# Optimization experiments

Measured on AMD Instinct MI355X. Metric: run time of the kernel, lower is better.

Reference implementation:

```python
import jax, jax.numpy as jnp
import numpy as np

HID = 256
E = 2 * HID  # 512, attention embed dim
H = 2        # attention heads


def _lin(x, w, b):
    return x @ w.T + b


def setup_inputs() -> dict:
    key = jax.random.key(0)
    ks = jax.random.split(key, 16)
    N, Ng, G = 65536, 4096, 16
    s = 0.02
    def w(k, o, i):
        return jax.random.normal(k, (o, i), jnp.float32) * s
    return {
        "flat_pair_enc": jax.random.normal(ks[0], (N, E), jnp.float32),
        "flat_pair_encA": jax.random.normal(ks[1], (N, E + 2), jnp.float32),
        "attn_in_w": w(ks[2], 3 * E, E), "attn_in_b": jnp.zeros(3 * E, jnp.float32),
        "attn_out_w": w(ks[3], E, E), "attn_out_b": jnp.zeros(E, jnp.float32),
        "phi1_w1": w(ks[4], HID, E + 2), "phi1_b1": jnp.zeros(HID, jnp.float32),
        "phi1_w2": w(ks[5], HID, HID), "phi1_b2": jnp.zeros(HID, jnp.float32),
        "phi1_w3": w(ks[6], HID, HID), "phi1_b3": jnp.zeros(HID, jnp.float32),
        "phi1_w4": w(ks[7], E, HID), "phi1_b4": jnp.zeros(E, jnp.float32),
        "g_w1": w(ks[8], HID, E), "g_b1": jnp.zeros(HID, jnp.float32),
        "g_w2": w(ks[9], HID, HID), "g_b2": jnp.zeros(HID, jnp.float32),
        "g_w3": w(ks[10], HID, HID), "g_b3": jnp.zeros(HID, jnp.float32),
        "g_w4": w(ks[11], 1, HID), "g_b4": jnp.zeros(1, jnp.float32),
        "phi2_w1": w(ks[12], HID, E), "phi2_b1": jnp.zeros(HID, jnp.float32),
        "phi2_w2": w(ks[13], HID, HID), "phi2_b2": jnp.zeros(HID, jnp.float32),
        "phi2_w3": w(ks[14], 2, HID), "phi2_b3": jnp.zeros(2, jnp.float32),
        "num_groups": 4096,
        "group_size": 16,
    }


def reference(flat_pair_enc, flat_pair_encA,
              attn_in_w, attn_in_b, attn_out_w, attn_out_b,
              phi1_w1, phi1_b1, phi1_w2, phi1_b2, phi1_w3, phi1_b3, phi1_w4, phi1_b4,
              g_w1, g_b1, g_w2, g_b2, g_w3, g_b3, g_w4, g_b4,
              phi2_w1, phi2_b1, phi2_w2, phi2_b2, phi2_w3, phi2_b3,
              num_groups, group_size):
    elu = jax.nn.elu
    Ng, G = num_groups, group_size
    # phi1 (note the double ELU after the second Linear, as in the source)
    h = elu(_lin(flat_pair_encA, phi1_w1, phi1_b1))
    h = elu(elu(_lin(h, phi1_w2, phi1_b2)))
    h = elu(_lin(h, phi1_w3, phi1_b3))
    key1 = _lin(h, phi1_w4, phi1_b4)                      # (N, E)
    x = key1.reshape(Ng, G, E)                            # segmented groups
    # per-group MultiheadAttention (torch semantics: packed in_proj, scale 1/sqrt(dh))
    qkv = x @ attn_in_w.T + attn_in_b                     # (Ng, G, 3E)
    q, k, v = jnp.split(qkv, 3, axis=-1)
    dh = E // H
    def heads(t):
        return t.reshape(Ng, G, H, dh).transpose(0, 2, 1, 3)  # (Ng, H, G, dh)
    q, k, v = heads(q), heads(k), heads(v)
    scores = jnp.einsum('nhqd,nhkd->nhqk', q, k) / jnp.sqrt(jnp.float32(dh))
    a = jax.nn.softmax(scores, axis=-1)
    o = jnp.einsum('nhqk,nhkd->nhqd', a, v).transpose(0, 2, 1, 3).reshape(Ng, G, E)
    key1_mean = (o @ attn_out_w.T + attn_out_b).mean(axis=1)  # (Ng, E) — mean over seq
    # g head
    hg = elu(_lin(key1_mean, g_w1, g_b1))
    hg = elu(_lin(hg, g_w2, g_b2))
    hg = elu(_lin(hg, g_w3, g_b3))
    q_jt = _lin(hg, g_w4, g_b4)                           # (Ng, 1)
    # alt values: k2 + kbar1 - key1/|g|  (counts per group == G)
    alt_val = flat_pair_enc.reshape(Ng, G, E) + key1_mean[:, None, :] - x / G
    hp = elu(_lin(alt_val, phi2_w1, phi2_b1))
    hp = elu(_lin(hp, phi2_w2, phi2_b2))
    alt_q = _lin(hp, phi2_w3, phi2_b3)                    # (Ng, G, 2)
    return (q_jt, alt_q)
```

## Files before the change

kernel.cpp:

```cpp
#include <hip/hip_runtime.h>
#include <cstdint>

typedef __bf16 bf16;
typedef __attribute__((ext_vector_type(8))) __bf16 bf16x8;
typedef __attribute__((ext_vector_type(4))) __bf16 bf16x4;
typedef __attribute__((ext_vector_type(4))) float f32x4;
typedef __attribute__((ext_vector_type(2))) float f32x2;

static __device__ __forceinline__ float elu1(float x) {
    return x > 0.f ? x : (__expf(x) - 1.f);
}

static __device__ __forceinline__ void gl_lds16(const void* gp, void* lp) {
    __builtin_amdgcn_global_load_lds(
        (const __attribute__((address_space(1))) void*)(uintptr_t)gp,
        (__attribute__((address_space(3))) void*)(uint32_t)(uintptr_t)lp,
        16, 0, 0);
}

struct CvtArgs {
    const float* src[13];
    int rows[13];
    int scols[13];
    int dcols[13];
    int total;
};

__global__ void cvt_k(CvtArgs a, bf16* __restrict__ dst) {
    int idx = blockIdx.x * 256 + threadIdx.x;
    if (idx >= a.total) return;
    int rem = idx;
#pragma unroll 1
    for (int s = 0; s < 13; ++s) {
        int sz = a.rows[s] * a.dcols[s];
        if (rem < sz) {
            int r = rem / a.dcols[s];
            int c = rem - r * a.dcols[s];
            float v = (c < a.scols[s]) ? a.src[s][(long)r * a.scols[s] + c] : 0.f;
            dst[idx] = (bf16)v;
            return;
        }
        rem -= sz;
    }
}

__global__ void cvtA_k(const float* __restrict__ src, bf16* __restrict__ dst) {
    const int idx = blockIdx.x * 256 + threadIdx.x;
    const int r = idx / 72;
    const int c8 = (idx - r * 72) * 8;
    const float* sp = src + (long)r * 514 + c8;
    bf16x8 t;
    if (c8 + 8 <= 514) {
        f32x2 p0 = *(const f32x2*)(sp + 0);
        f32x2 p1 = *(const f32x2*)(sp + 2);
        f32x2 p2 = *(const f32x2*)(sp + 4);
        f32x2 p3 = *(const f32x2*)(sp + 6);
        t[0] = (bf16)p0.x; t[1] = (bf16)p0.y; t[2] = (bf16)p1.x; t[3] = (bf16)p1.y;
        t[4] = (bf16)p2.x; t[5] = (bf16)p2.y; t[6] = (bf16)p3.x; t[7] = (bf16)p3.y;
    } else {
#pragma unroll
        for (int e = 0; e < 8; ++e) {
            const int col = c8 + e;
            t[e] = (bf16)(col < 514 ? sp[e] : 0.f);
        }
    }
    *(bf16x8*)(dst + (long)r * 576 + c8) = t;
}

struct GemmArgs {
    const float* Af;
    const bf16*  Ab;
    long lda;
    const float* enc;
    const float* km;
    const bf16*  key1;
    const bf16*  W;
    long ldw;
    const float* bias;
    bf16*  Cb;
    float* Cf;
    long ldc;
    int nK;
    int klim;
};

enum { AM_F32 = 0, AM_F32U = 1, AM_BF16 = 2, AM_ALT = 3 };
enum { ACT_NONE = 0, ACT_ELU = 1, ACT_ELU2 = 2 };

template <int AMODE, int ACT, bool OUTB>
__global__ __launch_bounds__(256, 2) void gemm_t(GemmArgs g) {
    __shared__ bf16 As[128 * 64];
    __shared__ bf16 Bs[128 * 64];

    const int tid  = threadIdx.x;
    const int wave = tid >> 6;
    const int lane = tid & 63;
    const int ln   = lane & 15;
    const int quad = lane >> 4;

    const long m0 = (long)blockIdx.x * 128;
    const long n0 = (long)blockIdx.y * 128;
    const int  wm = (wave & 1) * 64;
    const int  wn = (wave >> 1) * 64;

    f32x4 acc[4][4] = {};

    int cm[4], cs[4];
    long ar[4];
    if constexpr (AMODE != AM_BF16) {
#pragma unroll
        for (int r = 0; r < 4; ++r) {
            const int c = r * 256 + tid;
            cm[r] = c >> 3;
            cs[r] = c & 7;
            ar[r] = m0 + cm[r];
        }
    }

    f32x4 pf[4][2];
    float pu[4][8];
    f32x4 pe[4][2], pq[4][2];
    bf16x8 px[4];

    auto loadA = [&](int k0) {
#pragma unroll
        for (int r = 0; r < 4; ++r) {
            const int kk = k0 + (((cs[r] - cm[r]) & 7) << 3);
            if constexpr (AMODE == AM_F32) {
                const float* ap = g.Af + ar[r] * g.lda + kk;
                pf[r][0] = *(const f32x4*)ap;
                pf[r][1] = *(const f32x4*)(ap + 4);
            } else if constexpr (AMODE == AM_F32U) {
                const float* ap = g.Af + ar[r] * g.lda;
                if (kk + 8 <= g.klim) {
#pragma unroll
                    for (int e = 0; e < 8; e += 2) {
                        f32x2 p = *(const f32x2*)(ap + kk + e);
                        pu[r][e] = p.x;
                        pu[r][e + 1] = p.y;
                    }
                } else {
#pragma unroll
                    for (int e = 0; e < 8; ++e) {
                        const int col = kk + e;
                        pu[r][e] = col < g.klim ? ap[col] : 0.f;
                    }
                }
            } else if constexpr (AMODE == AM_ALT) {
                const float* ep = g.enc + ar[r] * 512 + kk;
                const float* mp = g.km + (ar[r] >> 4) * 512 + kk;
                pe[r][0] = *(const f32x4*)ep;
                pe[r][1] = *(const f32x4*)(ep + 4);
                pq[r][0] = *(const f32x4*)mp;
                pq[r][1] = *(const f32x4*)(mp + 4);
                px[r] = *(const bf16x8*)(g.key1 + ar[r] * 512 + kk);
            }
        }
    };

    auto writeA = [&]() {
#pragma unroll
        for (int r = 0; r < 4; ++r) {
            bf16x8 t;
            if constexpr (AMODE == AM_F32) {
#pragma unroll
                for (int e = 0; e < 4; ++e) {
                    t[e]     = (bf16)pf[r][0][e];
                    t[e + 4] = (bf16)pf[r][1][e];
                }
            } else if constexpr (AMODE == AM_F32U) {
#pragma unroll
                for (int e = 0; e < 8; ++e) t[e] = (bf16)pu[r][e];
            } else {
#pragma unroll
                for (int e = 0; e < 4; ++e) {
                    t[e]     = (bf16)(pe[r][0][e] + pq[r][0][e] - (float)px[r][e] * 0.0625f);
                    t[e + 4] = (bf16)(pe[r][1][e] + pq[r][1][e] - (float)px[r][e + 4] * 0.0625f);
                }
            }
            *(bf16x8*)(&As[cm[r] * 64 + cs[r] * 8]) = t;
        }
    };

    if constexpr (AMODE != AM_BF16) loadA(0);

    for (int ks = 0; ks < g.nK; ++ks) {
        const int k0 = ks * 64;
        __syncthreads();

        if constexpr (AMODE == AM_BF16) {
            const int cbase = wave * 256;
#pragma unroll
            for (int r = 0; r < 4; ++r) {
                const int c = cbase + r * 64 + lane;
                const int m = c >> 3, s = c & 7;
                const int pg = (s - m) & 7;
                gl_lds16(g.Ab + (m0 + m) * g.lda + k0 + pg * 8, &As[c * 8]);
            }
        } else {
            writeA();
        }

        {
            const int cbase = wave * 256;
#pragma unroll
            for (int r = 0; r < 4; ++r) {
                const int c = cbase + r * 64 + lane;
                const int n = c >> 3, s = c & 7;
                const int pg = (s - n) & 7;
                gl_lds16(g.W + (n0 + n) * g.ldw + k0 + pg * 8, &Bs[c * 8]);
            }
        }
        __syncthreads();

        if constexpr (AMODE != AM_BF16) {
            if (ks + 1 < g.nK) loadA(k0 + 64);
        }

#pragma unroll
        for (int ksub = 0; ksub < 2; ++ksub) {
            bf16x8 av[4], bv[4];
#pragma unroll
            for (int t = 0; t < 4; ++t) {
                const int m = wm + t * 16 + ln;
                const int sa = ((ksub * 4 + quad) + m) & 7;
                av[t] = *(const bf16x8*)(&As[m * 64 + sa * 8]);
                const int n = wn + t * 16 + ln;
                const int sb = ((ksub * 4 + quad) + n) & 7;
                bv[t] = *(const bf16x8*)(&Bs[n * 64 + sb * 8]);
            }
#pragma unroll
            for (int i = 0; i < 4; ++i)
#pragma unroll
                for (int j = 0; j < 4; ++j)
                    acc[i][j] = __builtin_amdgcn_mfma_f32_16x16x32_bf16(
                        av[i], bv[j], acc[i][j], 0, 0, 0);
        }
    }

#pragma unroll
    for (int i = 0; i < 4; ++i) {
        const long rb = m0 + wm + i * 16 + quad * 4;
#pragma unroll
        for (int j = 0; j < 4; ++j) {
            const long n = n0 + wn + j * 16 + ln;
            const float bvs = g.bias[n];
#pragma unroll
            for (int r = 0; r < 4; ++r) {
                float v = acc[i][j][r] + bvs;
                if constexpr (ACT >= ACT_ELU) v = elu1(v);
                if constexpr (ACT == ACT_ELU2) v = elu1(v);
                const long o = (rb + r) * g.ldc + n;
                if constexpr (OUTB) g.Cb[o] = (bf16)v;
                else                g.Cf[o] = v;
            }
        }
    }
}

__global__ __launch_bounds__(256) void attn_k(const bf16* __restrict__ qkv,
                                              bf16* __restrict__ obar,
                                              int ngroups) {
    const int tid = blockIdx.x * 256 + threadIdx.x;
    const int wv = tid >> 6;
    const int g  = wv >> 1;
    const int h  = wv & 1;
    if (g >= ngroups) return;
    const int lane = threadIdx.x & 63;
    const int i  = lane & 15;
    const int jb = (lane >> 4) << 2;

    const bf16* base  = qkv + (long)g * 16 * 1536;
    const bf16* qrow  = base + (long)i * 1536 + h * 256;
    const bf16* kbase = base + 512 + h * 256;

    float s0 = 0.f, s1 = 0.f, s2 = 0.f, s3 = 0.f;
    for (int kk = 0; kk < 256; kk += 8) {
        bf16x8 qv = *(const bf16x8*)(qrow + kk);
        float qf[8];
#pragma unroll
        for (int e = 0; e < 8; ++e) qf[e] = (float)qv[e];
        bf16x8 k0 = *(const bf16x8*)(kbase + (long)(jb + 0) * 1536 + kk);
        bf16x8 k1 = *(const bf16x8*)(kbase + (long)(jb + 1) * 1536 + kk);
        bf16x8 k2 = *(const bf16x8*)(kbase + (long)(jb + 2) * 1536 + kk);
        bf16x8 k3 = *(const bf16x8*)(kbase + (long)(jb + 3) * 1536 + kk);
#pragma unroll
        for (int e = 0; e < 8; ++e) {
            s0 += qf[e] * (float)k0[e];
            s1 += qf[e] * (float)k1[e];
            s2 += qf[e] * (float)k2[e];
            s3 += qf[e] * (float)k3[e];
        }
    }
    const float sc = 1.f / 16.f;
    s0 *= sc; s1 *= sc; s2 *= sc; s3 *= sc;
    float m = fmaxf(fmaxf(s0, s1), fmaxf(s2, s3));
    m = fmaxf(m, __shfl_xor(m, 16));
    m = fmaxf(m, __shfl_xor(m, 32));
    float e0 = __expf(s0 - m), e1 = __expf(s1 - m), e2 = __expf(s2 - m), e3 = __expf(s3 - m);
    float rs = e0 + e1 + e2 + e3;
    rs += __shfl_xor(rs, 16);
    rs += __shfl_xor(rs, 32);
    const float inv = 1.f / (rs * 16.f);
    float cb[4] = {e0 * inv, e1 * inv, e2 * inv, e3 * inv};
#pragma unroll
    for (int msk = 1; msk <= 8; msk <<= 1) {
        cb[0] += __shfl_xor(cb[0], msk);
        cb[1] += __shfl_xor(cb[1], msk);
        cb[2] += __shfl_xor(cb[2], msk);
        cb[3] += __shfl_xor(cb[3], msk);
    }
    float call[16];
#pragma unroll
    for (int j = 0; j < 16; ++j)
        call[j] = __shfl(cb[j & 3], (j >> 2) << 4);

    const int d0 = lane << 2;
    const bf16* vb = base + 1024 + h * 256 + d0;
    float o0 = 0.f, o1 = 0.f, o2 = 0.f, o3 = 0.f;
#pragma unroll
    for (int j = 0; j < 16; ++j) {
        bf16x4 vv = *(const bf16x4*)(vb + (long)j * 1536);
        o0 += call[j] * (float)vv[0];
        o1 += call[j] * (float)vv[1];
        o2 += call[j] * (float)vv[2];
        o3 += call[j] * (float)vv[3];
    }
    bf16x4 ov;
    ov[0] = (bf16)o0; ov[1] = (bf16)o1; ov[2] = (bf16)o2; ov[3] = (bf16)o3;
    *(bf16x4*)(obar + (long)g * 512 + h * 256 + d0) = ov;
}

__global__ void qjt_k(const bf16* __restrict__ hg, const bf16* __restrict__ w,
                      const float* __restrict__ b, float* __restrict__ out) {
    const int m = blockIdx.x * 256 + threadIdx.x;
    const bf16* hp = hg + (long)m * 256;
    float acc = 0.f;
    for (int k = 0; k < 256; k += 8) {
        bf16x8 hv = *(const bf16x8*)(hp + k);
        bf16x8 wv = *(const bf16x8*)(w + k);
#pragma unroll
        for (int e = 0; e < 8; ++e) acc += (float)hv[e] * (float)wv[e];
    }
    out[m] = acc + b[0];
}

__global__ void altq_k(const bf16* __restrict__ hp, const bf16* __restrict__ w,
                       const float* __restrict__ b, float* __restrict__ out) {
    const int m = blockIdx.x * 256 + threadIdx.x;
    const bf16* hr = hp + (long)m * 256;
    float a0 = 0.f, a1 = 0.f;
    for (int k = 0; k < 256; k += 8) {
        bf16x8 hv = *(const bf16x8*)(hr + k);
        bf16x8 w0 = *(const bf16x8*)(w + k);
        bf16x8 w1 = *(const bf16x8*)(w + 256 + k);
#pragma unroll
        for (int e = 0; e < 8; ++e) {
            float hf = (float)hv[e];
            a0 += hf * (float)w0[e];
            a1 += hf * (float)w1[e];
        }
    }
    out[2 * m]     = a0 + b[0];
    out[2 * m + 1] = a1 + b[1];
}

extern "C" void kernel_launch(void* const* d_in, const int* in_sizes, int n_in,
                              void* d_out, int out_size, void* d_ws, size_t ws_size,
                              hipStream_t stream) {
    const float* enc    = (const float*)d_in[0];
    const float* encA   = (const float*)d_in[1];
    const float* w_ain  = (const float*)d_in[2];
    const float* b_ain  = (const float*)d_in[3];
    const float* w_aout = (const float*)d_in[4];
    const float* b_aout = (const float*)d_in[5];
    const float* w_p11  = (const float*)d_in[6];
    const float* b_p11  = (const float*)d_in[7];
    const float* w_p12  = (const float*)d_in[8];
    const float* b_p12  = (const float*)d_in[9];
    const float* w_p13  = (const float*)d_in[10];
    const float* b_p13  = (const float*)d_in[11];
    const float* w_p14  = (const float*)d_in[12];
    const float* b_p14  = (const float*)d_in[13];
    const float* w_g1   = (const float*)d_in[14];
    const float* b_g1   = (const float*)d_in[15];
    const float* w_g2   = (const float*)d_in[16];
    const float* b_g2   = (const float*)d_in[17];
    const float* w_g3   = (const float*)d_in[18];
    const float* b_g3   = (const float*)d_in[19];
    const float* w_g4   = (const float*)d_in[20];
    const float* b_g4   = (const float*)d_in[21];
    const float* w_p21  = (const float*)d_in[22];
    const float* b_p21  = (const float*)d_in[23];
    const float* w_p22  = (const float*)d_in[24];
    const float* b_p22  = (const float*)d_in[25];
    const float* w_p23  = (const float*)d_in[26];
    const float* b_p23  = (const float*)d_in[27];
    float* out = (float*)d_out;

    char* wsc = (char*)d_ws;
    size_t off = 0;
    auto take = [&](size_t bytes) -> char* {
        char* p = wsc + off;
        off += (bytes + 255) & ~(size_t)255;
        return p;
    };

    const long o_ain  = 0;
    const long o_aout = o_ain + 1536L * 512;
    const long o_p11  = o_aout + 512L * 512;
    const long o_p12  = o_p11 + 256L * 576;
    const long o_p13  = o_p12 + 256L * 256;
    const long o_p14  = o_p13 + 256L * 256;
    const long o_g1   = o_p14 + 512L * 256;
    const long o_g2   = o_g1 + 256L * 512;
    const long o_g3   = o_g2 + 256L * 256;
    const long o_g4   = o_g3 + 256L * 256;
    const long o_p21  = o_g4 + 256L;
    const long o_p22  = o_p21 + 256L * 512;
    const long o_p23  = o_p22 + 256L * 256;
    const long wtot   = o_p23 + 2L * 256;

    bf16*  wb  = (bf16*)take((size_t)wtot * 2);
    bf16*  Ha  = (bf16*)take(65536ull * 256 * 2);
    bf16*  Hb  = (bf16*)take(65536ull * 256 * 2);
    bf16*  K1  = (bf16*)take(65536ull * 512 * 2);
    bf16*  OB  = (bf16*)take(4096ull * 512 * 2);
    float* KM  = (float*)take(4096ull * 512 * 4);
    bf16*  HGa = (bf16*)take(4096ull * 256 * 2);
    bf16*  HGb = (bf16*)take(4096ull * 256 * 2);

    const size_t apad_b = 65536ull * 576 * 2;
    const size_t avail = ws_size > off ? ws_size - off : 0;
    bool apad_ok = apad_b <= avail;
    auto qkvb = [](int ch) { return (size_t)(65536 / ch) * 1536 * 2; };
    auto need = [&](size_t q) {
        const size_t a = apad_ok ? apad_b : 0;
        return q > a ? q : a;
    };
    int CH = 16;
    if (need(qkvb(2)) <= avail)      CH = 2;
    else if (need(qkvb(4)) <= avail) CH = 4;
    else if (need(qkvb(8)) <= avail) CH = 8;
    else {
        CH = 16;
        if (need(qkvb(16)) > avail) apad_ok = false;
    }
    bf16* U = (bf16*)take(need(qkvb(CH)));
    bf16* Apad = U;
    bf16* QKV  = U;

    CvtArgs ca;
    const float* srcs[13] = {w_ain, w_aout, w_p11, w_p12, w_p13, w_p14,
                             w_g1, w_g2, w_g3, w_g4, w_p21, w_p22, w_p23};
    const int rows_[13]  = {1536, 512, 256, 256, 256, 512, 256, 256, 256, 1, 256, 256, 2};
    const int scols_[13] = {512, 512, 514, 256, 256, 256, 512, 256, 256, 256, 512, 256, 256};
    const int dcols_[13] = {512, 512, 576, 256, 256, 256, 512, 256, 256, 256, 512, 256, 256};
    for (int s = 0; s < 13; ++s) {
        ca.src[s] = srcs[s]; ca.rows[s] = rows_[s];
        ca.scols[s] = scols_[s]; ca.dcols[s] = dcols_[s];
    }
    ca.total = (int)wtot;
    cvt_k<<<dim3((unsigned)((wtot + 255) / 256)), dim3(256), 0, stream>>>(ca, wb);
    if (apad_ok)
        cvtA_k<<<dim3(18432), dim3(256), 0, stream>>>(encA, Apad);

    GemmArgs ga;

    if (apad_ok) {
        ga = {}; ga.Ab = Apad; ga.lda = 576;
        ga.W = wb + o_p11; ga.ldw = 576; ga.bias = b_p11;
        ga.Cb = Ha; ga.ldc = 256; ga.nK = 9;
        gemm_t<AM_BF16, ACT_ELU, true><<<dim3(512, 2), 256, 0, stream>>>(ga);
    } else {
        ga = {}; ga.Af = encA; ga.lda = 514; ga.klim = 514;
        ga.W = wb + o_p11; ga.ldw = 576; ga.bias = b_p11;
        ga.Cb = Ha; ga.ldc = 256; ga.nK = 9;
        gemm_t<AM_F32U, ACT_ELU, true><<<dim3(512, 2), 256, 0, stream>>>(ga);
    }

    ga = {}; ga.Ab = Ha; ga.lda = 256; ga.W = wb + o_p12; ga.ldw = 256;
    ga.bias = b_p12; ga.Cb = Hb; ga.ldc = 256; ga.nK = 4;
    gemm_t<AM_BF16, ACT_ELU2, true><<<dim3(512, 2), 256, 0, stream>>>(ga);

    ga = {}; ga.Ab = Hb; ga.lda = 256; ga.W = wb + o_p13; ga.ldw = 256;
    ga.bias = b_p13; ga.Cb = Ha; ga.ldc = 256; ga.nK = 4;
    gemm_t<AM_BF16, ACT_ELU, true><<<dim3(512, 2), 256, 0, stream>>>(ga);

    ga = {}; ga.Ab = Ha; ga.lda = 256; ga.W = wb + o_p14; ga.ldw = 256;
    ga.bias = b_p14; ga.Cb = K1; ga.ldc = 512; ga.nK = 4;
    gemm_t<AM_BF16, ACT_NONE, true><<<dim3(512, 4), 256, 0, stream>>>(ga);

    const int Mc = 65536 / CH;
    const int gc = 4096 / CH;
    for (int c = 0; c < CH; ++c) {
        ga = {}; ga.Ab = K1 + (long)c * Mc * 512; ga.lda = 512;
        ga.W = wb + o_ain; ga.ldw = 512; ga.bias = b_ain;
        ga.Cb = QKV; ga.ldc = 1536; ga.nK = 8;
        gemm_t<AM_BF16, ACT_NONE, true>
            <<<dim3(Mc / 128, 12), 256, 0, stream>>>(ga);
        attn_k<<<dim3((gc * 2) / 4), 256, 0, stream>>>(QKV, OB + (long)c * gc * 512, gc);
    }

    ga = {}; ga.Ab = OB; ga.lda = 512; ga.W = wb + o_aout; ga.ldw = 512;
    ga.bias = b_aout; ga.Cf = KM; ga.ldc = 512; ga.nK = 8;
    gemm_t<AM_BF16, ACT_NONE, false><<<dim3(32, 4), 256, 0, stream>>>(ga);

    ga = {}; ga.Af = KM; ga.lda = 512; ga.W = wb + o_g1; ga.ldw = 512;
    ga.bias = b_g1; ga.Cb = HGa; ga.ldc = 256; ga.nK = 8;
    gemm_t<AM_F32, ACT_ELU, true><<<dim3(32, 2), 256, 0, stream>>>(ga);

    ga = {}; ga.Ab = HGa; ga.lda = 256; ga.W = wb + o_g2; ga.ldw = 256;
    ga.bias = b_g2; ga.Cb = HGb; ga.ldc = 256; ga.nK = 4;
    gemm_t<AM_BF16, ACT_ELU, true><<<dim3(32, 2), 256, 0, stream>>>(ga);

    ga = {}; ga.Ab = HGb; ga.lda = 256; ga.W = wb + o_g3; ga.ldw = 256;
    ga.bias = b_g3; ga.Cb = HGa; ga.ldc = 256; ga.nK = 4;
    gemm_t<AM_BF16, ACT_ELU, true><<<dim3(32, 2), 256, 0, stream>>>(ga);

    qjt_k<<<dim3(16), 256, 0, stream>>>(HGa, wb + o_g4, b_g4, out);

    ga = {}; ga.enc = enc; ga.km = KM; ga.key1 = K1;
    ga.W = wb + o_p21; ga.ldw = 512; ga.bias = b_p21;
    ga.Cb = Ha; ga.ldc = 256; ga.nK = 8;
    gemm_t<AM_ALT, ACT_ELU, true><<<dim3(512, 2), 256, 0, stream>>>(ga);

    ga = {}; ga.Ab = Ha; ga.lda = 256; ga.W = wb + o_p22; ga.ldw = 256;
    ga.bias = b_p22; ga.Cb = Hb; ga.ldc = 256; ga.nK = 4;
    gemm_t<AM_BF16, ACT_ELU, true><<<dim3(512, 2), 256, 0, stream>>>(ga);

    altq_k<<<dim3(256), 256, 0, stream>>>(Hb, wb + o_p23, b_p23, out + 4096);
}
```

Baseline: 787.5 us.

## Double-buffer LDS tiles in GEMM to overlap loads with MFMA

```diff
diff --git a/kernel.cpp b/kernel.cpp
--- a/kernel.cpp
+++ b/kernel.cpp
@@ -89,8 +89,8 @@
 
 template <int AMODE, int ACT, bool OUTB>
 __global__ __launch_bounds__(256, 2) void gemm_t(GemmArgs g) {
-    __shared__ bf16 As[128 * 64];
-    __shared__ bf16 Bs[128 * 64];
+    __shared__ bf16 As[2][128 * 64];
+    __shared__ bf16 Bs[2][128 * 64];
 
     const int tid  = threadIdx.x;
     const int wave = tid >> 6;
@@ -158,7 +158,7 @@
         }
     };
 
-    auto writeA = [&]() {
+    auto writeA = [&](int b) {
 #pragma unroll
         for (int r = 0; r < 4; ++r) {
             bf16x8 t;
@@ -178,43 +178,59 @@
                     t[e + 4] = (bf16)(pe[r][1][e] + pq[r][1][e] - (float)px[r][e + 4] * 0.0625f);
                 }
             }
-            *(bf16x8*)(&As[cm[r] * 64 + cs[r] * 8]) = t;
+            *(bf16x8*)(&As[b][cm[r] * 64 + cs[r] * 8]) = t;
         }
     };
 
-    if constexpr (AMODE != AM_BF16) loadA(0);
-
+    auto stageA = [&](int ks, int b) {
+        const int cbase = wave * 256;
+        const int k0 = ks * 64;
+#pragma unroll
+        for (int r = 0; r < 4; ++r) {
+            const int c = cbase + r * 64 + lane;
+            const int m = c >> 3, s = c & 7;
+            const int pg = (s - m) & 7;
+            gl_lds16(g.Ab + (m0 + m) * g.lda + k0 + pg * 8, &As[b][c * 8]);
+        }
+    };
+
+    auto stageB = [&](int ks, int b) {
+        const int cbase = wave * 256;
+        const int k0 = ks * 64;
+#pragma unroll
+        for (int r = 0; r < 4; ++r) {
+            const int c = cbase + r * 64 + lane;
+            const int n = c >> 3, s = c & 7;
+            const int pg = (s - n) & 7;
+            gl_lds16(g.W + (n0 + n) * g.ldw + k0 + pg * 8, &Bs[b][c * 8]);
+        }
+    };
+
+    if constexpr (AMODE == AM_BF16) {
+        stageA(0, 0);
+    } else {
+        loadA(0);
+        writeA(0);
+    }
+    stageB(0, 0);
+    if constexpr (AMODE != AM_BF16) {
+        if (g.nK > 1) loadA(64);
+    }
+
+    int cur = 0;
     for (int ks = 0; ks < g.nK; ++ks) {
-        const int k0 = ks * 64;
         __syncthreads();
 
-        if constexpr (AMODE == AM_BF16) {
-            const int cbase = wave * 256;
-#pragma unroll
-            for (int r = 0; r < 4; ++r) {
-                const int c = cbase + r * 64 + lane;
-                const int m = c >> 3, s = c & 7;
-                const int pg = (s - m) & 7;
-                gl_lds16(g.Ab + (m0 + m) * g.lda + k0 + pg * 8, &As[c * 8]);
+        if (ks + 1 < g.nK) {
+            if constexpr (AMODE == AM_BF16) {
+                stageA(ks + 1, cur ^ 1);
+            } else {
+                writeA(cur ^ 1);
             }
-        } else {
-            writeA();
-        }
-
-        {
-            const int cbase = wave * 256;
-#pragma unroll
-            for (int r = 0; r < 4; ++r) {
-                const int c = cbase + r * 64 + lane;
-                const int n = c >> 3, s = c & 7;
-                const int pg = (s - n) & 7;
-                gl_lds16(g.W + (n0 + n) * g.ldw + k0 + pg * 8, &Bs[c * 8]);
+            stageB(ks + 1, cur ^ 1);
+            if constexpr (AMODE != AM_BF16) {
+                if (ks + 2 < g.nK) loadA((ks + 2) * 64);
             }
-        }
-        __syncthreads();
-
-        if constexpr (AMODE != AM_BF16) {
-            if (ks + 1 < g.nK) loadA(k0 + 64);
         }
 
 #pragma unroll
@@ -224,10 +240,10 @@
             for (int t = 0; t < 4; ++t) {
                 const int m = wm + t * 16 + ln;
                 const int sa = ((ksub * 4 + quad) + m) & 7;
-                av[t] = *(const bf16x8*)(&As[m * 64 + sa * 8]);
+                av[t] = *(const bf16x8*)(&As[cur][m * 64 + sa * 8]);
                 const int n = wn + t * 16 + ln;
                 const int sb = ((ksub * 4 + quad) + n) & 7;
-                bv[t] = *(const bf16x8*)(&Bs[n * 64 + sb * 8]);
+                bv[t] = *(const bf16x8*)(&Bs[cur][n * 64 + sb * 8]);
             }
 #pragma unroll
             for (int i = 0; i < 4; ++i)
@@ -236,6 +252,7 @@
                     acc[i][j] = __builtin_amdgcn_mfma_f32_16x16x32_bf16(
                         av[i], bv[j], acc[i][j], 0, 0, 0);
         }
+        cur ^= 1;
     }
 
 #pragma unroll
```

Measured after the change: 810.0 us. 2.9% more time.

## Double-buffer GEMM LDS tiles to overlap next-tile staging with MFMA compute

Applied to the files above, without the earlier changes.

```diff
diff --git a/kernel.cpp b/kernel.cpp
--- a/kernel.cpp
+++ b/kernel.cpp
@@ -89,8 +89,10 @@
 
 template <int AMODE, int ACT, bool OUTB>
 __global__ __launch_bounds__(256, 2) void gemm_t(GemmArgs g) {
-    __shared__ bf16 As[128 * 64];
-    __shared__ bf16 Bs[128 * 64];
+    __shared__ bf16 As0[128 * 64];
+    __shared__ bf16 As1[128 * 64];
+    __shared__ bf16 Bs0[128 * 64];
+    __shared__ bf16 Bs1[128 * 64];
 
     const int tid  = threadIdx.x;
     const int wave = tid >> 6;
@@ -158,7 +160,7 @@
         }
     };
 
-    auto writeA = [&]() {
+    auto writeA = [&](bf16 (&Ad)[128 * 64]) {
 #pragma unroll
         for (int r = 0; r < 4; ++r) {
             bf16x8 t;
@@ -178,45 +180,35 @@
                     t[e + 4] = (bf16)(pe[r][1][e] + pq[r][1][e] - (float)px[r][e + 4] * 0.0625f);
                 }
             }
-            *(bf16x8*)(&As[cm[r] * 64 + cs[r] * 8]) = t;
-        }
-    };
-
-    if constexpr (AMODE != AM_BF16) loadA(0);
-
-    for (int ks = 0; ks < g.nK; ++ks) {
+            *(bf16x8*)(&Ad[cm[r] * 64 + cs[r] * 8]) = t;
+        }
+    };
+
+    auto stageA = [&](int ks, bf16 (&Ad)[128 * 64]) {
+        const int cbase = wave * 256;
         const int k0 = ks * 64;
-        __syncthreads();
-
-        if constexpr (AMODE == AM_BF16) {
-            const int cbase = wave * 256;
-#pragma unroll
-            for (int r = 0; r < 4; ++r) {
-                const int c = cbase + r * 64 + lane;
-                const int m = c >> 3, s = c & 7;
-                const int pg = (s - m) & 7;
-                gl_lds16(g.Ab + (m0 + m) * g.lda + k0 + pg * 8, &As[c * 8]);
-            }
-        } else {
-            writeA();
-        }
-
-        {
-            const int cbase = wave * 256;
-#pragma unroll
-            for (int r = 0; r < 4; ++r) {
-                const int c = cbase + r * 64 + lane;
-                const int n = c >> 3, s = c & 7;
-                const int pg = (s - n) & 7;
-                gl_lds16(g.W + (n0 + n) * g.ldw + k0 + pg * 8, &Bs[c * 8]);
-            }
-        }
-        __syncthreads();
-
-        if constexpr (AMODE != AM_BF16) {
-            if (ks + 1 < g.nK) loadA(k0 + 64);
-        }
-
+#pragma unroll
+        for (int r = 0; r < 4; ++r) {
+            const int c = cbase + r * 64 + lane;
+            const int m = c >> 3, s = c & 7;
+            const int pg = (s - m) & 7;
+            gl_lds16(g.Ab + (m0 + m) * g.lda + k0 + pg * 8, &Ad[c * 8]);
+        }
+    };
+
+    auto stageB = [&](int ks, bf16 (&Bd)[128 * 64]) {
+        const int cbase = wave * 256;
+        const int k0 = ks * 64;
+#pragma unroll
+        for (int r = 0; r < 4; ++r) {
+            const int c = cbase + r * 64 + lane;
+            const int n = c >> 3, s = c & 7;
+            const int pg = (s - n) & 7;
+            gl_lds16(g.W + (n0 + n) * g.ldw + k0 + pg * 8, &Bd[c * 8]);
+        }
+    };
+
+    auto computeT = [&](const bf16 (&Ab_)[128 * 64], const bf16 (&Bb_)[128 * 64]) {
 #pragma unroll
         for (int ksub = 0; ksub < 2; ++ksub) {
             bf16x8 av[4], bv[4];
@@ -224,10 +216,10 @@
             for (int t = 0; t < 4; ++t) {
                 const int m = wm + t * 16 + ln;
                 const int sa = ((ksub * 4 + quad) + m) & 7;
-                av[t] = *(const bf16x8*)(&As[m * 64 + sa * 8]);
+                av[t] = *(const bf16x8*)(&Ab_[m * 64 + sa * 8]);
                 const int n = wn + t * 16 + ln;
                 const int sb = ((ksub * 4 + quad) + n) & 7;
-                bv[t] = *(const bf16x8*)(&Bs[n * 64 + sb * 8]);
+                bv[t] = *(const bf16x8*)(&Bb_[n * 64 + sb * 8]);
             }
 #pragma unroll
             for (int i = 0; i < 4; ++i)
@@ -236,6 +228,44 @@
                     acc[i][j] = __builtin_amdgcn_mfma_f32_16x16x32_bf16(
                         av[i], bv[j], acc[i][j], 0, 0, 0);
         }
+    };
+
+    if constexpr (AMODE == AM_BF16) {
+        stageA(0, As0);
+    } else {
+        loadA(0);
+        writeA(As0);
+    }
+    stageB(0, Bs0);
+    if constexpr (AMODE != AM_BF16) {
+        if (g.nK > 1) loadA(64);
+    }
+
+    const int nK = g.nK;
+    for (int ks = 0;;) {
+        __syncthreads();
+        if (ks + 1 < nK) {
+            if constexpr (AMODE == AM_BF16) stageA(ks + 1, As1);
+            else                            writeA(As1);
+            stageB(ks + 1, Bs1);
+            if constexpr (AMODE != AM_BF16) {
+                if (ks + 2 < nK) loadA((ks + 2) * 64);
+            }
+        }
+        computeT(As0, Bs0);
+        if (++ks >= nK) break;
+
+        __syncthreads();
+        if (ks + 1 < nK) {
+            if constexpr (AMODE == AM_BF16) stageA(ks + 1, As0);
+            else                            writeA(As0);
+            stageB(ks + 1, Bs0);
+            if constexpr (AMODE != AM_BF16) {
+                if (ks + 2 < nK) loadA((ks + 2) * 64);
+            }
+        }
+        computeT(As1, Bs1);
+        if (++ks >= nK) break;
     }
 
 #pragma unroll
```

Measured after the change: 887.2 us. 1.13x slower.
